# Kernel optimization log

Hardware: AMD Instinct MI355X
Metric: run time of the kernel (lower is better)

The kernel has to match this reference:

```python
import jax, jax.numpy as jnp
import numpy as np

T, B, H = 512, 256, 512

def setup_inputs() -> dict:
    key = jax.random.key(0)
    k1, k2, k3, k4 = jax.random.split(key, 4)
    scale = 1.0 / np.sqrt(H)
    return {
        "ins": jax.random.normal(k1, (T, B, H), dtype=jnp.float32),
        "resets": jax.random.bernoulli(k2, 0.05, (T, B)),
        "Wi": jax.random.normal(k3, (H, 3 * H), dtype=jnp.float32) * scale,
        "bi": jnp.zeros((3 * H,), dtype=jnp.float32),
        "Wh": jax.random.normal(k4, (H, 3 * H), dtype=jnp.float32) * scale,
        "bhn": jnp.zeros((H,), dtype=jnp.float32),
    }

def reference(ins, resets, Wi, bi, Wh, bhn):
    # GRU scan with per-step reset masking (flax GRUCell math).
    h0 = jnp.zeros((B, H), dtype=ins.dtype)

    def step(h, xs):
        x_t, r_t = xs  # x_t: [B,H], r_t: [B] bool
        h = jnp.where(r_t[:, None], 0.0, h)
        gi = x_t @ Wi + bi            # [B,3H] : ir | iz | in
        gh = h @ Wh                   # [B,3H] : hr | hz | hn
        xr, xz, xn = jnp.split(gi, 3, axis=-1)
        hr, hz, hn = jnp.split(gh, 3, axis=-1)
        r = jax.nn.sigmoid(xr + hr)
        z = jax.nn.sigmoid(xz + hz)
        n = jnp.tanh(xn + r * (hn + bhn))
        h_new = (1.0 - z) * n + z * h
        return h_new, h_new

    _, ys = jax.lax.scan(step, h0, (ins, resets))
    return ys  # [T,B,H]
```

## Files before the change

kernel.cpp:

```cpp
#include <hip/hip_runtime.h>
#include <hip/hip_bf16.h>

#define T_STEPS 512
#define B_SZ    256
#define H_SZ    512
#define G3      1536
#define EX_DW   (B_SZ * H_SZ / 2)
#define NSLOT   4

typedef __attribute__((ext_vector_type(8))) short short8;
typedef __attribute__((ext_vector_type(4))) int   int4v;
typedef __attribute__((ext_vector_type(4))) float f32x4;

__device__ unsigned int g_cnt[T_STEPS * 8];
__device__ float        g_keep[(T_STEPS + 1) * B_SZ];
__device__ unsigned int g_exch[NSLOT * EX_DW];

__device__ __forceinline__ unsigned short f2b(float f) {
    return __builtin_bit_cast(unsigned short, __float2bfloat16(f));
}

__global__ void prep_kernel(const unsigned char* __restrict__ resets_raw) {
    __shared__ int s_isbyte;
    const int tid = threadIdx.x;
    if (tid == 0) s_isbyte = 0;

    for (int i = tid; i < T_STEPS * 8; i += 1024)
        __hip_atomic_store(&g_cnt[i], 0u, __ATOMIC_RELAXED, __HIP_MEMORY_SCOPE_SYSTEM);
    __syncthreads();

    const int n = T_STEPS * B_SZ;
    int found = 0;
    for (int i = tid; i < n; i += 1024) {
        if ((i & 3) && resets_raw[i]) found = 1;
    }
    if (found) s_isbyte = 1;
    __syncthreads();
    const int isbyte = s_isbyte;

    const int* ri = (const int*)resets_raw;
    for (int i = tid; i < n; i += 1024) {
        bool r = isbyte ? (resets_raw[i] != 0) : (ri[i] != 0);
        g_keep[i] = r ? 0.0f : 1.0f;
    }
    for (int i = tid; i < B_SZ; i += 1024) g_keep[n + i] = 0.0f;
}

__launch_bounds__(384, 1)
__global__ void gru_main(const float* __restrict__ ins,
                         const float* __restrict__ Wi,
                         const float* __restrict__ bi,
                         const float* __restrict__ Wh,
                         const float* __restrict__ bhn,
                         float* __restrict__ out) {
    __shared__ __align__(16) unsigned short lWi[3 * 16 * 64 * 8];
    __shared__ __align__(16) unsigned short lWh[3 * 16 * 64 * 8];
    __shared__ __align__(16) unsigned short sHb[2 * 16 * 64 * 8];
    __shared__ float sGi[32 * 48];
    __shared__ float sGh[32 * 48];
    __shared__ float sHp[32 * 16];
    __shared__ float sBi[48];
    __shared__ float sBhn[16];

    const int tid  = threadIdx.x;
    const int pb   = blockIdx.x & 7;
    const int pc   = blockIdx.x >> 3;
    const int r0   = pb * 32;
    const int c0   = pc * 16;
    const int lane = tid & 63;
    const int w    = tid >> 6;
    const int mt   = (w >= 3) ? 1 : 0;
    const int nt   = w - mt * 3;

    for (int idx = tid; idx < 3 * 16 * 64; idx += 384) {
        int snt = idx >> 10, skt = (idx >> 6) & 15, sl = idx & 63;
        int col = snt * 512 + c0 + (sl & 15);
        int kb  = skt * 32 + ((sl >> 4) << 3);
#pragma unroll
        for (int j = 0; j < 8; ++j) {
            lWi[idx * 8 + j] = f2b(Wi[(size_t)(kb + j) * G3 + col]);
            lWh[idx * 8 + j] = f2b(Wh[(size_t)(kb + j) * G3 + col]);
        }
    }
    if (tid < 48) sBi[tid]  = bi[(tid >> 4) * 512 + c0 + (tid & 15)];
    if (tid < 16) sBhn[tid] = bhn[c0 + tid];
    for (int i = tid; i < 512; i += 384) sHp[i] = 0.0f;
    __syncthreads();

    const int grow  = r0 + mt * 16 + (lane & 15);
    const int koff  = (lane >> 4) << 3;
    const int ccol  = lane & 15;
    const int crow0 = (mt << 4) + ((lane >> 4) << 2);

    const short8* wip = (const short8*)lWi + nt * 16 * 64 + lane;
    const short8* whp = (const short8*)lWh + nt * 16 * 64 + lane;
    const short8* hbp = (const short8*)sHb + mt * 16 * 64 + lane;
    short8*       hbw = (short8*)sHb       + mt * 16 * 64 + lane;

    const bool loader = (nt == 0);

    f32x4 acc_gi = {0.f, 0.f, 0.f, 0.f};
    {
        const float* xrow = ins + (size_t)grow * H_SZ + koff;
#pragma unroll
        for (int kt = 0; kt < 16; ++kt) {
            const f32x4* p = (const f32x4*)(xrow + kt * 32);
            f32x4 x0 = p[0], x1 = p[1];
            short8 a;
#pragma unroll
            for (int j = 0; j < 4; ++j) { a[j] = (short)f2b(x0[j]); a[4 + j] = (short)f2b(x1[j]); }
            acc_gi = __builtin_amdgcn_mfma_f32_16x16x32_bf16(a, wip[kt * 64], acc_gi, 0, 0, 0);
        }
    }

    for (int t = 0; t < T_STEPS; ++t) {
        if (t > 0 && loader) {
            unsigned int* cp = &g_cnt[(t - 1) * 8 + pb];
            int guard = 0;
            while (__hip_atomic_load(cp, __ATOMIC_RELAXED, __HIP_MEMORY_SCOPE_SYSTEM) < 32u) {
                __builtin_amdgcn_s_sleep(1);
                if (++guard > (1 << 22)) break;
            }
            asm volatile("" ::: "memory");
            const char* ebase = (const char*)g_exch
                + (size_t)((t - 1) & (NSLOT - 1)) * (EX_DW * 4)
                + (size_t)grow * (H_SZ * 2) + koff * 2;
            int4v hf[16];
#pragma unroll
            for (int kt = 0; kt < 16; ++kt)
                asm volatile("global_load_dwordx4 %0, %1, off sc0 sc1"
                             : "=v"(hf[kt]) : "v"(ebase + kt * 64));
            asm volatile("s_waitcnt vmcnt(0)" ::: "memory");
            __builtin_amdgcn_sched_barrier(0);
#pragma unroll
            for (int kt = 0; kt < 16; ++kt)
                hbw[kt * 64] = __builtin_bit_cast(short8, hf[kt]);
        }
        __syncthreads();

        f32x4 acch = {0.f, 0.f, 0.f, 0.f};
        if (t > 0) {
#pragma unroll
            for (int kt = 0; kt < 16; ++kt)
                acch = __builtin_amdgcn_mfma_f32_16x16x32_bf16(hbp[kt * 64], whp[kt * 64], acch, 0, 0, 0);
        }

#pragma unroll
        for (int rg = 0; rg < 4; ++rg) {
            sGi[(crow0 + rg) * 48 + nt * 16 + ccol] = acc_gi[rg];
            sGh[(crow0 + rg) * 48 + nt * 16 + ccol] = acch[rg];
        }
        __syncthreads();

        if (tid < 256) {
            const int row = tid >> 3;
            const int j0  = (tid & 7) * 2;
            const int gr  = r0 + row;
            float hv[2];
#pragma unroll
            for (int u = 0; u < 2; ++u) {
                const int j = j0 + u;
                const float xr = sGi[row * 48 + j]      + sBi[j];
                const float xz = sGi[row * 48 + 16 + j] + sBi[16 + j];
                const float xn = sGi[row * 48 + 32 + j] + sBi[32 + j];
                const float hr = sGh[row * 48 + j];
                const float hz = sGh[row * 48 + 16 + j];
                const float hn = sGh[row * 48 + 32 + j];
                const float rg = 1.f / (1.f + __expf(-(xr + hr)));
                const float zg = 1.f / (1.f + __expf(-(xz + hz)));
                float targ = xn + rg * (hn + sBhn[j]);
                targ = fminf(15.f, fmaxf(-15.f, targ));
                const float e2 = __expf(-2.f * targ);
                const float ng = (1.f - e2) / (1.f + e2);
                const float hp = sHp[row * 16 + j];
                hv[u] = (1.f - zg) * ng + zg * hp;
            }
            *(float2*)(out + ((size_t)t * B_SZ + gr) * H_SZ + c0 + j0) = make_float2(hv[0], hv[1]);
            const float kn  = g_keep[(t + 1) * B_SZ + gr];
            const float hm0 = hv[0] * kn, hm1 = hv[1] * kn;
            sHp[row * 16 + j0]     = hm0;
            sHp[row * 16 + j0 + 1] = hm1;
            const unsigned int pk = (unsigned int)f2b(hm0) | ((unsigned int)f2b(hm1) << 16);
            __hip_atomic_store(&g_exch[(t & (NSLOT - 1)) * EX_DW + gr * 256 + (c0 >> 1) + (tid & 7)],
                               pk, __ATOMIC_RELAXED, __HIP_MEMORY_SCOPE_SYSTEM);
        }
        asm volatile("s_waitcnt vmcnt(0)" ::: "memory");
        __syncthreads();
        if (tid == 0)
            __hip_atomic_fetch_add(&g_cnt[t * 8 + pb], 1u,
                                   __ATOMIC_RELAXED, __HIP_MEMORY_SCOPE_SYSTEM);

        if (t + 1 < T_STEPS) {
            const float* xrow = ins + ((size_t)(t + 1) * B_SZ + grow) * H_SZ + koff;
            f32x4 ag = {0.f, 0.f, 0.f, 0.f};
#pragma unroll
            for (int kt = 0; kt < 16; ++kt) {
                const f32x4* p = (const f32x4*)(xrow + kt * 32);
                f32x4 x0 = p[0], x1 = p[1];
                short8 a;
#pragma unroll
                for (int j = 0; j < 4; ++j) { a[j] = (short)f2b(x0[j]); a[4 + j] = (short)f2b(x1[j]); }
                ag = __builtin_amdgcn_mfma_f32_16x16x32_bf16(a, wip[kt * 64], ag, 0, 0, 0);
            }
            acc_gi = ag;
        }
    }
}

extern "C" void kernel_launch(void* const* d_in, const int* in_sizes, int n_in,
                              void* d_out, int out_size, void* d_ws, size_t ws_size,
                              hipStream_t stream) {
    const float* ins    = (const float*)d_in[0];
    const void*  resets = d_in[1];
    const float* Wi     = (const float*)d_in[2];
    const float* bi     = (const float*)d_in[3];
    const float* Wh     = (const float*)d_in[4];
    const float* bhn    = (const float*)d_in[5];
    float*       outp   = (float*)d_out;

    prep_kernel<<<1, 1024, 0, stream>>>((const unsigned char*)resets);
    gru_main<<<256, 384, 0, stream>>>(ins, Wi, bi, Wh, bhn, outp);
}
```

Measured before the change: 4.558 ms.

## Replace counter barrier with tagged 16-byte hidden-state packets polled directly

Removes the per-step global atomic counter and spin-wait. Each block now writes its bf16 hidden-state slice as self-validating 16-byte records, with a launch-id and step tag in the first dword. Consumers poll those records directly, which removes the separate flag round-trip and the store-drain wait before signalling. All threads now share the loading instead of one wave, and the exchange uses two slots with a padded LDS layout. The cost is more polled global traffic, and correctness now rests on 16-byte stores being seen atomically.

After: 4.375 ms. 1.04x faster.

```diff
diff --git a/kernel.cpp b/kernel.cpp
--- a/kernel.cpp
+++ b/kernel.cpp
@@ -5,16 +5,19 @@
 #define B_SZ    256
 #define H_SZ    512
 #define G3      1536
-#define EX_DW   (B_SZ * H_SZ / 2)
-#define NSLOT   4
+
+#define CH_ROW      96
+#define ROW_BYTES   (CH_ROW * 16)
+#define SLOT_BYTES  (B_SZ * ROW_BYTES)
+#define HR_STRIDE   520
 
 typedef __attribute__((ext_vector_type(8))) short short8;
 typedef __attribute__((ext_vector_type(4))) int   int4v;
 typedef __attribute__((ext_vector_type(4))) float f32x4;
 
-__device__ unsigned int g_cnt[T_STEPS * 8];
+__device__ unsigned int g_launch;
 __device__ float        g_keep[(T_STEPS + 1) * B_SZ];
-__device__ unsigned int g_exch[NSLOT * EX_DW];
+__device__ __align__(16) unsigned int g_exch[2 * SLOT_BYTES / 4];
 
 __device__ __forceinline__ unsigned short f2b(float f) {
     return __builtin_bit_cast(unsigned short, __float2bfloat16(f));
@@ -23,17 +26,16 @@
 __global__ void prep_kernel(const unsigned char* __restrict__ resets_raw) {
     __shared__ int s_isbyte;
     const int tid = threadIdx.x;
-    if (tid == 0) s_isbyte = 0;
-
-    for (int i = tid; i < T_STEPS * 8; i += 1024)
-        __hip_atomic_store(&g_cnt[i], 0u, __ATOMIC_RELAXED, __HIP_MEMORY_SCOPE_SYSTEM);
+    if (tid == 0) {
+        s_isbyte = 0;
+        __hip_atomic_fetch_add(&g_launch, 1u, __ATOMIC_RELAXED, __HIP_MEMORY_SCOPE_SYSTEM);
+    }
     __syncthreads();
 
     const int n = T_STEPS * B_SZ;
     int found = 0;
-    for (int i = tid; i < n; i += 1024) {
+    for (int i = tid; i < n; i += 1024)
         if ((i & 3) && resets_raw[i]) found = 1;
-    }
     if (found) s_isbyte = 1;
     __syncthreads();
     const int isbyte = s_isbyte;
@@ -55,12 +57,14 @@
                          float* __restrict__ out) {
     __shared__ __align__(16) unsigned short lWi[3 * 16 * 64 * 8];
     __shared__ __align__(16) unsigned short lWh[3 * 16 * 64 * 8];
-    __shared__ __align__(16) unsigned short sHb[2 * 16 * 64 * 8];
+    __shared__ __align__(16) unsigned short sHr[32 * HR_STRIDE];
     __shared__ float sGi[32 * 48];
     __shared__ float sGh[32 * 48];
     __shared__ float sHp[32 * 16];
+    __shared__ unsigned int sHx[32 * 8];
     __shared__ float sBi[48];
     __shared__ float sBhn[16];
+    __shared__ unsigned sLid;
 
     const int tid  = threadIdx.x;
     const int pb   = blockIdx.x & 7;
@@ -72,6 +76,14 @@
     const int mt   = (w >= 3) ? 1 : 0;
     const int nt   = w - mt * 3;
 
+    if (tid == 0) {
+        unsigned lid_;
+        const void* lp = (const void*)&g_launch;
+        asm volatile("global_load_dword %0, %1, off sc0 sc1" : "=v"(lid_) : "v"(lp) : "memory");
+        asm volatile("s_waitcnt vmcnt(0)" ::: "memory");
+        sLid = lid_;
+    }
+
     for (int idx = tid; idx < 3 * 16 * 64; idx += 384) {
         int snt = idx >> 10, skt = (idx >> 6) & 15, sl = idx & 63;
         int col = snt * 512 + c0 + (sl & 15);
@@ -86,18 +98,31 @@
     if (tid < 16) sBhn[tid] = bhn[c0 + tid];
     for (int i = tid; i < 512; i += 384) sHp[i] = 0.0f;
     __syncthreads();
-
-    const int grow  = r0 + mt * 16 + (lane & 15);
-    const int koff  = (lane >> 4) << 3;
+    const unsigned lid = sLid;
+
+    const int grow = r0 + mt * 16 + (lane & 15);
+    const int koff = (lane >> 4) << 3;
     const int ccol  = lane & 15;
     const int crow0 = (mt << 4) + ((lane >> 4) << 2);
 
     const short8* wip = (const short8*)lWi + nt * 16 * 64 + lane;
     const short8* whp = (const short8*)lWh + nt * 16 * 64 + lane;
-    const short8* hbp = (const short8*)sHb + mt * 16 * 64 + lane;
-    short8*       hbw = (short8*)sHb       + mt * 16 * 64 + lane;
-
-    const bool loader = (nt == 0);
+    const short8* hfp = (const short8*)(sHr + (mt * 16 + (lane & 15)) * HR_STRIDE + koff);
+
+    unsigned gofs[8], ldo[8];
+    bool ldn[8];
+#pragma unroll
+    for (int i = 0; i < 8; ++i) {
+        const int q = tid + 384 * i;
+        const int row = q / 96, g = q % 96;
+        const int colbase = (g / 3) * 16 + (g % 3) * 6;
+        gofs[i] = (unsigned)(((r0 + row) * 96 + g) * 16);
+        ldo[i]  = (unsigned)(row * HR_STRIDE + colbase);
+        ldn[i]  = ((g % 3) < 2);
+    }
+    const int prow = tid / 3;
+    const int pc3  = tid % 3;
+    const size_t pofs = ((size_t)(r0 + prow) * 96 + pc * 3 + pc3) * 16;
 
     f32x4 acc_gi = {0.f, 0.f, 0.f, 0.f};
     {
@@ -114,27 +139,41 @@
     }
 
     for (int t = 0; t < T_STEPS; ++t) {
-        if (t > 0 && loader) {
-            unsigned int* cp = &g_cnt[(t - 1) * 8 + pb];
+        if (t > 0) {
+            const unsigned want = (lid << 10) | (unsigned)t;
+            const char* abase = (const char*)g_exch + (size_t)((t - 1) & 1) * SLOT_BYTES;
+            int4v cv[8];
+            unsigned pend = 0xFFu;
+#pragma unroll
+            for (int i = 0; i < 8; ++i) {
+                const char* ap = abase + gofs[i];
+                asm volatile("global_load_dwordx4 %0, %1, off sc0 sc1" : "=v"(cv[i]) : "v"(ap) : "memory");
+            }
             int guard = 0;
-            while (__hip_atomic_load(cp, __ATOMIC_RELAXED, __HIP_MEMORY_SCOPE_SYSTEM) < 32u) {
-                __builtin_amdgcn_s_sleep(1);
+            for (;;) {
+                asm volatile("s_waitcnt vmcnt(0)" ::: "memory");
+#pragma unroll
+                for (int i = 0; i < 8; ++i) {
+                    if ((pend >> i) & 1u) {
+                        if ((unsigned)cv[i][0] == want) {
+                            unsigned* lp = (unsigned*)(sHr + ldo[i]);
+                            lp[0] = (unsigned)cv[i][1];
+                            lp[1] = (unsigned)cv[i][2];
+                            if (ldn[i]) lp[2] = (unsigned)cv[i][3];
+                            pend &= ~(1u << i);
+                        }
+                    }
+                }
+                if (!pend) break;
                 if (++guard > (1 << 22)) break;
-            }
-            asm volatile("" ::: "memory");
-            const char* ebase = (const char*)g_exch
-                + (size_t)((t - 1) & (NSLOT - 1)) * (EX_DW * 4)
-                + (size_t)grow * (H_SZ * 2) + koff * 2;
-            int4v hf[16];
-#pragma unroll
-            for (int kt = 0; kt < 16; ++kt)
-                asm volatile("global_load_dwordx4 %0, %1, off sc0 sc1"
-                             : "=v"(hf[kt]) : "v"(ebase + kt * 64));
-            asm volatile("s_waitcnt vmcnt(0)" ::: "memory");
-            __builtin_amdgcn_sched_barrier(0);
-#pragma unroll
-            for (int kt = 0; kt < 16; ++kt)
-                hbw[kt * 64] = __builtin_bit_cast(short8, hf[kt]);
+#pragma unroll
+                for (int i = 0; i < 8; ++i) {
+                    if ((pend >> i) & 1u) {
+                        const char* ap = abase + gofs[i];
+                        asm volatile("global_load_dwordx4 %0, %1, off sc0 sc1" : "=v"(cv[i]) : "v"(ap) : "memory");
+                    }
+                }
+            }
         }
         __syncthreads();
 
@@ -142,7 +181,7 @@
         if (t > 0) {
 #pragma unroll
             for (int kt = 0; kt < 16; ++kt)
-                acch = __builtin_amdgcn_mfma_f32_16x16x32_bf16(hbp[kt * 64], whp[kt * 64], acch, 0, 0, 0);
+                acch = __builtin_amdgcn_mfma_f32_16x16x32_bf16(hfp[kt * 4], whp[kt * 64], acch, 0, 0, 0);
         }
 
 #pragma unroll
@@ -180,15 +219,20 @@
             const float hm0 = hv[0] * kn, hm1 = hv[1] * kn;
             sHp[row * 16 + j0]     = hm0;
             sHp[row * 16 + j0 + 1] = hm1;
-            const unsigned int pk = (unsigned int)f2b(hm0) | ((unsigned int)f2b(hm1) << 16);
-            __hip_atomic_store(&g_exch[(t & (NSLOT - 1)) * EX_DW + gr * 256 + (c0 >> 1) + (tid & 7)],
-                               pk, __ATOMIC_RELAXED, __HIP_MEMORY_SCOPE_SYSTEM);
-        }
-        asm volatile("s_waitcnt vmcnt(0)" ::: "memory");
+            sHx[row * 8 + (tid & 7)] = (unsigned)f2b(hm0) | ((unsigned)f2b(hm1) << 16);
+        }
         __syncthreads();
-        if (tid == 0)
-            __hip_atomic_fetch_add(&g_cnt[t * 8 + pb], 1u,
-                                   __ATOMIC_RELAXED, __HIP_MEMORY_SCOPE_SYSTEM);
+
+        if (t + 1 < T_STEPS && tid < 96) {
+            const unsigned tag = (lid << 10) | (unsigned)(t + 1);
+            const unsigned p0 = sHx[prow * 8 + pc3 * 3];
+            const unsigned p1 = sHx[prow * 8 + pc3 * 3 + 1];
+            const unsigned p2 = (pc3 < 2) ? sHx[prow * 8 + pc3 * 3 + 2] : 0u;
+            int4v d;
+            d[0] = (int)tag; d[1] = (int)p0; d[2] = (int)p1; d[3] = (int)p2;
+            const char* ap = (const char*)g_exch + (size_t)(t & 1) * SLOT_BYTES + pofs;
+            asm volatile("global_store_dwordx4 %0, %1, off sc0 sc1" :: "v"(ap), "v"(d) : "memory");
+        }
 
         if (t + 1 < T_STEPS) {
             const float* xrow = ins + ((size_t)(t + 1) * B_SZ + grow) * H_SZ + koff;
```
